# Optimization experiments

Hardware: AMD Instinct MI355X
Metric: run time of the kernel (lower is better)

## Reference

```python
import jax, jax.numpy as jnp
import numpy as np

B, H, W, C, D = 8, 64, 64, 128, 16


def setup_inputs() -> dict:
    key = jax.random.key(0)
    ks = jax.random.split(key, 6)
    scale = 1.0 / np.sqrt(C)
    return {
        "x": jax.random.normal(ks[0], (B, H, W, C), dtype=jnp.float32),
        "w_f": jax.random.normal(ks[1], (C, D), dtype=jnp.float32) * scale,
        "w_g": jax.random.normal(ks[2], (C, D), dtype=jnp.float32) * scale,
        "w_h": jax.random.normal(ks[3], (C, D), dtype=jnp.float32) * scale,
        "w_v": jax.random.normal(ks[4], (D, C), dtype=jnp.float32) * (1.0 / np.sqrt(D)),
        "gamma": jax.random.normal(ks[5], (1,), dtype=jnp.float32) * 0.1,
    }


def reference(x, w_f, w_g, w_h, w_v, gamma):
    b, h, w, c = x.shape
    n = h * w
    xf = x.reshape(b, n, c)                      # flatten spatial dims
    f = jnp.einsum('bnc,cd->bnd', xf, w_f)       # 1x1 conv == channel matmul
    g = jnp.einsum('bnc,cd->bnd', xf, w_g)
    hh = jnp.einsum('bnc,cd->bnd', xf, w_h)
    scores = jnp.einsum('bnd,bmd->bnm', f, g)    # [B, N, N], no 1/sqrt(d) scaling (faithful)
    attn = jax.nn.softmax(scores, axis=1)        # NOTE: softmax over axis=1 as in original
    y = jnp.einsum('bnm,bmd->bnd', attn, hh)     # [B, N, D]
    y = jnp.einsum('bnd,dc->bnc', y, w_v)        # output 1x1 conv
    y = y.reshape(b, h, w, c)
    return gamma * y + x
```

## Files before the change

kernel.cpp:

```cpp
#include <hip/hip_runtime.h>

typedef _Float16 f16;
typedef _Float16 f16x4 __attribute__((ext_vector_type(4)));
typedef _Float16 n16x2 __attribute__((ext_vector_type(2)));
typedef float    f32x4 __attribute__((ext_vector_type(4)));

#define LOG2E 1.44269504088896340736f
#define OFF25 36.0673760222824936f

__device__ __forceinline__ f32x4 MFMA(f16x4 a, f16x4 b, f32x4 c) {
#if defined(__HIP_DEVICE_COMPILE__)
    return __builtin_amdgcn_mfma_f32_16x16x16f16(a, b, c, 0, 0, 0);
#else
    return c;
#endif
}

__device__ __forceinline__ float fexp2(float x) {
#if defined(__HIP_DEVICE_COMPILE__)
    return __builtin_amdgcn_exp2f(x);
#else
    return exp2f(x);
#endif
}

__device__ __forceinline__ float flog2(float x) {
#if defined(__HIP_DEVICE_COMPILE__)
    return __builtin_amdgcn_logf(x);
#else
    return log2f(x);
#endif
}

__device__ __forceinline__ f16x4 pk4(float a, float b, float c, float d) {
#if defined(__HIP_DEVICE_COMPILE__)
    n16x2 lo = __builtin_bit_cast(n16x2, __builtin_amdgcn_cvt_pkrtz(a, b));
    n16x2 hi = __builtin_bit_cast(n16x2, __builtin_amdgcn_cvt_pkrtz(c, d));
    f16x4 r; r[0] = lo[0]; r[1] = lo[1]; r[2] = hi[0]; r[3] = hi[1];
    return r;
#else
    f16x4 r; r[0] = (f16)a; r[1] = (f16)b; r[2] = (f16)c; r[3] = (f16)d;
    return r;
#endif
}

__global__ __launch_bounds__(256) void k_proj(const float* __restrict__ x,
        const float* __restrict__ wf, const float* __restrict__ wg,
        const float* __restrict__ wh, f16* __restrict__ F,
        f16* __restrict__ G, f16* __restrict__ Hf) {
    const int lane = threadIdx.x & 63;
    const int wid  = threadIdx.x >> 6;
    const int tile = wid >> 1;
    const int kh   = wid & 1;
    const int g16  = lane >> 4;
    const int c16  = lane & 15;
    const long r0  = ((long)blockIdx.x * 2 + tile) * 16;

    f16x4 bw[3][4];
    const float* Ws[3] = { wf, wg, wh };
    #pragma unroll
    for (int w = 0; w < 3; ++w)
        #pragma unroll
        for (int kk = 0; kk < 4; ++kk) {
            const int kb = (kh * 4 + kk) * 16 + g16 * 4;
            bw[w][kk] = pk4(Ws[w][(kb + 0) * 16 + c16], Ws[w][(kb + 1) * 16 + c16],
                            Ws[w][(kb + 2) * 16 + c16], Ws[w][(kb + 3) * 16 + c16]);
        }

    f32x4 af = {0,0,0,0}, ag = {0,0,0,0}, ah = {0,0,0,0};
    const float* xr = x + (r0 + c16) * 128;
    #pragma unroll
    for (int kk = 0; kk < 4; ++kk) {
        float4 xa = *(const float4*)(xr + (kh * 4 + kk) * 16 + g16 * 4);
        f16x4 a = pk4(xa.x, xa.y, xa.z, xa.w);
        af = MFMA(a, bw[0][kk], af);
        ag = MFMA(a, bw[1][kk], ag);
        ah = MFMA(a, bw[2][kk], ah);
    }

    __shared__ float red[2][64][13];
    if (kh == 1) {
        #pragma unroll
        for (int i = 0; i < 4; ++i) {
            red[tile][lane][i]     = af[i];
            red[tile][lane][4 + i] = ag[i];
            red[tile][lane][8 + i] = ah[i];
        }
    }
    __syncthreads();
    if (kh == 0) {
        #pragma unroll
        for (int i = 0; i < 4; ++i) {
            af[i] += red[tile][lane][i];
            ag[i] += red[tile][lane][4 + i];
            ah[i] += red[tile][lane][8 + i];
        }
        #pragma unroll
        for (int i = 0; i < 4; ++i) {
            const long row = r0 + g16 * 4 + i;
            F[row * 16 + c16] = (f16)(af[i] * LOG2E);
            G[row * 16 + c16] = (f16)ag[i];
        }
        *(f16x4*)(Hf + (r0 >> 4) * 256 + lane * 4) =
            pk4(ah[0], ah[1], ah[2], ah[3]);
    }
}

__global__ __launch_bounds__(512) void k_cs(const f16* __restrict__ F,
        const f16* __restrict__ G, float* __restrict__ nM2) {
    const int lane = threadIdx.x & 63;
    const int tp   = threadIdx.x >> 6;
    const int b    = blockIdx.x >> 6;
    const int mb   = (blockIdx.x & 63) * 64;
    const int g16  = lane >> 4, c16 = lane & 15;
    const long bb  = (long)b * 4096;

    f16x4 ga[4];
    #pragma unroll
    for (int j = 0; j < 4; ++j)
        ga[j] = *(const f16x4*)(G + (bb + mb + 16 * j + c16) * 16 + g16 * 4);

    const f16* Fb = F + (bb + tp * 512) * 16;
    float zs[4][4];
    #pragma unroll
    for (int j = 0; j < 4; ++j)
        #pragma unroll
        for (int i = 0; i < 4; ++i) zs[j][i] = 0.f;

    const f32x4 coff = {-OFF25, -OFF25, -OFF25, -OFF25};
    f16x4 fb0 = *(const f16x4*)(Fb + (c16) * 16 + g16 * 4);
    f16x4 fb1 = *(const f16x4*)(Fb + (16 + c16) * 16 + g16 * 4);
    f16x4 fb2 = *(const f16x4*)(Fb + (32 + c16) * 16 + g16 * 4);
    for (int t = 0; t < 32; ++t) {
        f16x4 fbn = *(const f16x4*)(Fb + ((t + 3) * 16 + c16) * 16 + g16 * 4);
        #pragma unroll
        for (int j = 0; j < 4; ++j) {
            f32x4 s = MFMA(ga[j], fb0, coff);
            #pragma unroll
            for (int i = 0; i < 4; ++i)
                zs[j][i] += fexp2(s[i]);
        }
        fb0 = fb1; fb1 = fb2; fb2 = fbn;
    }
    #pragma unroll
    for (int d = 8; d >= 1; d >>= 1)
        #pragma unroll
        for (int j = 0; j < 4; ++j)
            #pragma unroll
            for (int i = 0; i < 4; ++i)
                zs[j][i] += __shfl_xor(zs[j][i], d);

    __shared__ float lz[8][64];
    if (c16 == 0) {
        #pragma unroll
        for (int j = 0; j < 4; ++j)
            #pragma unroll
            for (int i = 0; i < 4; ++i)
                lz[tp][16 * j + 4 * g16 + i] = zs[j][i];
    }
    __syncthreads();
    if (threadIdx.x < 64) {
        const int ml = threadIdx.x;
        float z = 0.f;
        #pragma unroll
        for (int p = 0; p < 8; ++p) z += lz[p][ml];
        nM2[bb + mb + ml] = -flog2(z) - OFF25;
    }
}

__global__ __launch_bounds__(512) void k_pv(const f16* __restrict__ F,
        const f16* __restrict__ G, const f16* __restrict__ Hf,
        const float* __restrict__ nM2, const float* __restrict__ wv,
        const float* __restrict__ xin, const float* __restrict__ gamma,
        float* __restrict__ out) {
    const int lane = threadIdx.x & 63;
    const int tp   = threadIdx.x >> 6;
    const int b    = blockIdx.x >> 6;
    const int n0   = (blockIdx.x & 63) * 64;
    const int g16  = lane >> 4, c16 = lane & 15;
    const long bb  = (long)b * 4096;

    f16x4 fbv[4];
    #pragma unroll
    for (int j = 0; j < 4; ++j)
        fbv[j] = *(const f16x4*)(F + (bb + n0 + 16 * j + c16) * 16 + g16 * 4);

    const int jo = tp >> 1, th = tp & 1;
    const float gm = gamma[0];
    f16x4 wvf[4];
    #pragma unroll
    for (int t = 0; t < 4; ++t) {
        const int c0 = (4 * th + t) * 16;
        wvf[t] = pk4(wv[(g16 * 4 + 0) * 128 + c0 + c16] * gm,
                     wv[(g16 * 4 + 1) * 128 + c0 + c16] * gm,
                     wv[(g16 * 4 + 2) * 128 + c0 + c16] * gm,
                     wv[(g16 * 4 + 3) * 128 + c0 + c16] * gm);
    }

    const f16* Gp = G + bb * 16;
    const f16* Hp = Hf + bb * 16 + lane * 4;
    const float* Np = nM2 + bb;
    const int mbase = tp * 512;

    f32x4 yT[4] = {{0,0,0,0},{0,0,0,0},{0,0,0,0},{0,0,0,0}};
    f16x4 ga0 = *(const f16x4*)(Gp + (mbase + c16) * 16 + g16 * 4);
    f16x4 ha0 = *(const f16x4*)(Hp + (long)mbase * 16);
    f32x4 nm0 = *(const f32x4*)(Np + mbase + g16 * 4);
    f16x4 ga1 = *(const f16x4*)(Gp + (mbase + 16 + c16) * 16 + g16 * 4);
    f16x4 ha1 = *(const f16x4*)(Hp + (long)(mbase + 16) * 16);
    f32x4 nm1 = *(const f32x4*)(Np + mbase + 16 + g16 * 4);
    f16x4 ga2 = *(const f16x4*)(Gp + (mbase + 32 + c16) * 16 + g16 * 4);
    f16x4 ha2 = *(const f16x4*)(Hp + (long)(mbase + 32) * 16);
    f32x4 nm2 = *(const f32x4*)(Np + mbase + 32 + g16 * 4);
    for (int t = 0; t < 32; ++t) {
        const int m3 = mbase + t * 16 + 48;
        f16x4 gan = *(const f16x4*)(Gp + (m3 + c16) * 16 + g16 * 4);
        f16x4 han = *(const f16x4*)(Hp + (long)m3 * 16);
        f32x4 nmn = *(const f32x4*)(Np + m3 + g16 * 4);
        #pragma unroll
        for (int j = 0; j < 4; ++j) {
            f32x4 s = MFMA(ga0, fbv[j], nm0);
            f16x4 pb = pk4(fexp2(s[0]), fexp2(s[1]),
                           fexp2(s[2]), fexp2(s[3]));
            yT[j] = MFMA(ha0, pb, yT[j]);
        }
        ga0 = ga1; ha0 = ha1; nm0 = nm1;
        ga1 = ga2; ha1 = ha2; nm1 = nm2;
        ga2 = gan; ha2 = han; nm2 = nmn;
    }

    __shared__ float red[8][4][64][5];
    #pragma unroll
    for (int j = 0; j < 4; ++j)
        #pragma unroll
        for (int i = 0; i < 4; ++i) red[tp][j][lane][i] = yT[j][i];
    __syncthreads();

    f32x4 ys = {0,0,0,0};
    #pragma unroll
    for (int p = 0; p < 8; ++p)
        #pragma unroll
        for (int i = 0; i < 4; ++i) ys[i] += red[p][jo][lane][i];
    const f16x4 ya = pk4(ys[0], ys[1], ys[2], ys[3]);

    #pragma unroll
    for (int t = 0; t < 4; ++t) {
        const int c0 = (4 * th + t) * 16;
        f32x4 zero = {0,0,0,0};
        f32x4 o = MFMA(ya, wvf[t], zero);
        #pragma unroll
        for (int i = 0; i < 4; ++i) {
            const long idx = (bb + n0 + 16 * jo + 4 * g16 + i) * 128 + c0 + c16;
            out[idx] = o[i] + xin[idx];
        }
    }
}

extern "C" void kernel_launch(void* const* d_in, const int* in_sizes, int n_in,
                              void* d_out, int out_size, void* d_ws, size_t ws_size,
                              hipStream_t stream) {
    const float* x     = (const float*)d_in[0];
    const float* wf    = (const float*)d_in[1];
    const float* wg    = (const float*)d_in[2];
    const float* wh    = (const float*)d_in[3];
    const float* wv    = (const float*)d_in[4];
    const float* gamma = (const float*)d_in[5];
    float* out = (float*)d_out;

    char* p = (char*)d_ws;
    const long BN  = 8L * 4096;
    const long PAD = 8192;
    f16*   F   = (f16*)p;    p += BN * 16 * sizeof(f16) + PAD;
    f16*   G   = (f16*)p;    p += BN * 16 * sizeof(f16) + PAD;
    f16*   Hf  = (f16*)p;    p += BN * 16 * sizeof(f16) + PAD;
    float* nM2 = (float*)p;  p += BN * sizeof(float)    + PAD;

    k_proj<<<1024, 256, 0, stream>>>(x, wf, wg, wh, F, G, Hf);
    k_cs  <<<512,  512, 0, stream>>>(F, G, nM2);
    k_pv  <<<512,  512, 0, stream>>>(F, G, Hf, nM2, wv, x, gamma, out);
}
```

Measured before the change: 51.37 us.

## Double waves per block in softmax-stat and PV kernels, splitting key range finer

Both the column-sum kernel and the attention-output kernel now launch 1024 threads (16 waves) per block instead of 512, each wave covering 256 keys instead of 512. The prefetch depth drops from three tiles to two. In the PV kernel the cross-wave reduction becomes a two-stage shared-memory add so the existing buffer can be reused, and the output projection is split over four wave quarters instead of two. The aim is more waves in flight per CU to hide latency on the 512-block grid. The cost is an extra barrier, shallower prefetch, and possible register pressure under the larger launch bound.

```diff
diff --git a/kernel.cpp b/kernel.cpp
--- a/kernel.cpp
+++ b/kernel.cpp
@@ -106,7 +106,7 @@
     }
 }
 
-__global__ __launch_bounds__(512) void k_cs(const f16* __restrict__ F,
+__global__ __launch_bounds__(1024) void k_cs(const f16* __restrict__ F,
         const f16* __restrict__ G, float* __restrict__ nM2) {
     const int lane = threadIdx.x & 63;
     const int tp   = threadIdx.x >> 6;
@@ -120,7 +120,7 @@
     for (int j = 0; j < 4; ++j)
         ga[j] = *(const f16x4*)(G + (bb + mb + 16 * j + c16) * 16 + g16 * 4);
 
-    const f16* Fb = F + (bb + tp * 512) * 16;
+    const f16* Fb = F + (bb + tp * 256) * 16;
     float zs[4][4];
     #pragma unroll
     for (int j = 0; j < 4; ++j)
@@ -130,9 +130,8 @@
     const f32x4 coff = {-OFF25, -OFF25, -OFF25, -OFF25};
     f16x4 fb0 = *(const f16x4*)(Fb + (c16) * 16 + g16 * 4);
     f16x4 fb1 = *(const f16x4*)(Fb + (16 + c16) * 16 + g16 * 4);
-    f16x4 fb2 = *(const f16x4*)(Fb + (32 + c16) * 16 + g16 * 4);
-    for (int t = 0; t < 32; ++t) {
-        f16x4 fbn = *(const f16x4*)(Fb + ((t + 3) * 16 + c16) * 16 + g16 * 4);
+    for (int t = 0; t < 16; ++t) {
+        f16x4 fbn = *(const f16x4*)(Fb + ((t + 2) * 16 + c16) * 16 + g16 * 4);
         #pragma unroll
         for (int j = 0; j < 4; ++j) {
             f32x4 s = MFMA(ga[j], fb0, coff);
@@ -140,7 +139,7 @@
             for (int i = 0; i < 4; ++i)
                 zs[j][i] += fexp2(s[i]);
         }
-        fb0 = fb1; fb1 = fb2; fb2 = fbn;
+        fb0 = fb1; fb1 = fbn;
     }
     #pragma unroll
     for (int d = 8; d >= 1; d >>= 1)
@@ -150,7 +149,7 @@
             for (int i = 0; i < 4; ++i)
                 zs[j][i] += __shfl_xor(zs[j][i], d);
 
-    __shared__ float lz[8][64];
+    __shared__ float lz[16][64];
     if (c16 == 0) {
         #pragma unroll
         for (int j = 0; j < 4; ++j)
@@ -163,12 +162,12 @@
         const int ml = threadIdx.x;
         float z = 0.f;
         #pragma unroll
-        for (int p = 0; p < 8; ++p) z += lz[p][ml];
+        for (int p = 0; p < 16; ++p) z += lz[p][ml];
         nM2[bb + mb + ml] = -flog2(z) - OFF25;
     }
 }
 
-__global__ __launch_bounds__(512) void k_pv(const f16* __restrict__ F,
+__global__ __launch_bounds__(1024) void k_pv(const f16* __restrict__ F,
         const f16* __restrict__ G, const f16* __restrict__ Hf,
         const float* __restrict__ nM2, const float* __restrict__ wv,
         const float* __restrict__ xin, const float* __restrict__ gamma,
@@ -185,12 +184,12 @@
     for (int j = 0; j < 4; ++j)
         fbv[j] = *(const f16x4*)(F + (bb + n0 + 16 * j + c16) * 16 + g16 * 4);
 
-    const int jo = tp >> 1, th = tp & 1;
+    const int jo = tp >> 2, tq = tp & 3;
     const float gm = gamma[0];
-    f16x4 wvf[4];
-    #pragma unroll
-    for (int t = 0; t < 4; ++t) {
-        const int c0 = (4 * th + t) * 16;
+    f16x4 wvf[2];
+    #pragma unroll
+    for (int t = 0; t < 2; ++t) {
+        const int c0 = (tq * 2 + t) * 16;
         wvf[t] = pk4(wv[(g16 * 4 + 0) * 128 + c0 + c16] * gm,
                      wv[(g16 * 4 + 1) * 128 + c0 + c16] * gm,
                      wv[(g16 * 4 + 2) * 128 + c0 + c16] * gm,
@@ -200,7 +199,7 @@
     const f16* Gp = G + bb * 16;
     const f16* Hp = Hf + bb * 16 + lane * 4;
     const float* Np = nM2 + bb;
-    const int mbase = tp * 512;
+    const int mbase = tp * 256;
 
     f32x4 yT[4] = {{0,0,0,0},{0,0,0,0},{0,0,0,0},{0,0,0,0}};
     f16x4 ga0 = *(const f16x4*)(Gp + (mbase + c16) * 16 + g16 * 4);
@@ -209,14 +208,11 @@
     f16x4 ga1 = *(const f16x4*)(Gp + (mbase + 16 + c16) * 16 + g16 * 4);
     f16x4 ha1 = *(const f16x4*)(Hp + (long)(mbase + 16) * 16);
     f32x4 nm1 = *(const f32x4*)(Np + mbase + 16 + g16 * 4);
-    f16x4 ga2 = *(const f16x4*)(Gp + (mbase + 32 + c16) * 16 + g16 * 4);
-    f16x4 ha2 = *(const f16x4*)(Hp + (long)(mbase + 32) * 16);
-    f32x4 nm2 = *(const f32x4*)(Np + mbase + 32 + g16 * 4);
-    for (int t = 0; t < 32; ++t) {
-        const int m3 = mbase + t * 16 + 48;
-        f16x4 gan = *(const f16x4*)(Gp + (m3 + c16) * 16 + g16 * 4);
-        f16x4 han = *(const f16x4*)(Hp + (long)m3 * 16);
-        f32x4 nmn = *(const f32x4*)(Np + m3 + g16 * 4);
+    for (int t = 0; t < 16; ++t) {
+        const int m2 = mbase + t * 16 + 32;
+        f16x4 gan = *(const f16x4*)(Gp + (m2 + c16) * 16 + g16 * 4);
+        f16x4 han = *(const f16x4*)(Hp + (long)m2 * 16);
+        f32x4 nmn = *(const f32x4*)(Np + m2 + g16 * 4);
         #pragma unroll
         for (int j = 0; j < 4; ++j) {
             f32x4 s = MFMA(ga0, fbv[j], nm0);
@@ -225,15 +221,24 @@
             yT[j] = MFMA(ha0, pb, yT[j]);
         }
         ga0 = ga1; ha0 = ha1; nm0 = nm1;
-        ga1 = ga2; ha1 = ha2; nm1 = nm2;
-        ga2 = gan; ha2 = han; nm2 = nmn;
+        ga1 = gan; ha1 = han; nm1 = nmn;
     }
 
     __shared__ float red[8][4][64][5];
-    #pragma unroll
-    for (int j = 0; j < 4; ++j)
-        #pragma unroll
-        for (int i = 0; i < 4; ++i) red[tp][j][lane][i] = yT[j][i];
+    if (tp >= 8) {
+        #pragma unroll
+        for (int j = 0; j < 4; ++j)
+            #pragma unroll
+            for (int i = 0; i < 4; ++i) red[tp - 8][j][lane][i] = yT[j][i];
+    }
+    __syncthreads();
+    if (tp < 8) {
+        #pragma unroll
+        for (int j = 0; j < 4; ++j)
+            #pragma unroll
+            for (int i = 0; i < 4; ++i)
+                red[tp][j][lane][i] += yT[j][i];
+    }
     __syncthreads();
 
     f32x4 ys = {0,0,0,0};
@@ -244,8 +249,8 @@
     const f16x4 ya = pk4(ys[0], ys[1], ys[2], ys[3]);
 
     #pragma unroll
-    for (int t = 0; t < 4; ++t) {
-        const int c0 = (4 * th + t) * 16;
+    for (int t = 0; t < 2; ++t) {
+        const int c0 = (tq * 2 + t) * 16;
         f32x4 zero = {0,0,0,0};
         f32x4 o = MFMA(ya, wvf[t], zero);
         #pragma unroll
@@ -275,7 +280,7 @@
     f16*   Hf  = (f16*)p;    p += BN * 16 * sizeof(f16) + PAD;
     float* nM2 = (float*)p;  p += BN * sizeof(float)    + PAD;
 
-    k_proj<<<1024, 256, 0, stream>>>(x, wf, wg, wh, F, G, Hf);
-    k_cs  <<<512,  512, 0, stream>>>(F, G, nM2);
-    k_pv  <<<512,  512, 0, stream>>>(F, G, Hf, nM2, wv, x, gamma, out);
-}
+    k_proj<<<1024, 256,  0, stream>>>(x, wf, wg, wh, F, G, Hf);
+    k_cs  <<<512,  1024, 0, stream>>>(F, G, nM2);
+    k_pv  <<<512,  1024, 0, stream>>>(F, G, Hf, nM2, wv, x, gamma, out);
+}
```

New measurement: 69.36 us. +35.0%, slower.
